# Performance work log

Hardware: AMD Instinct MI355X
Metric: run time of the kernel (lower is better)

Reference implementation:

```python
import jax, jax.numpy as jnp
import numpy as np

# Module config (mirrors SWTLayer(__init__) with dimensions=[64,64,16], kmax=[3,3], wavelet='db1')
DIMS = (64, 64)      # spatial sizes along axes 1,2
LEVELS = (6, 6)      # pywt.dwt_max_level(64, dec_len=2) == 6 (Haar)
KMAX = (3, 3)
NLIFT = 16
BATCH = 32


def swt_haar(x, level, axis):
    """pywt.swt(x, 'db1', level, trim_approx=True, norm=True) along `axis` (periodic).
    norm=True Haar level-j step s=2^(j-1): cA[i]=(a[i]+a[i+s])/2, cD[i]=(a[i]-a[i+s])/2.
    Returns concat([cA_n, cD_n, ..., cD_1]) along axis (length (level+1)*M)."""
    a = x
    details = []
    for j in range(level):
        s = 2 ** j
        sh = jnp.roll(a, -s, axis)   # a[i + s] (periodic)
        details.append((a - sh) * 0.5)
        a = (a + sh) * 0.5
    return jnp.concatenate([a] + details[::-1], axis=axis)


def iswt_haar(xt, level, axis):
    """pywt.iswt inverse of swt_haar: averages the two phase reconstructions per level."""
    bands = jnp.split(xt, level + 1, axis=axis)  # [cA_n, cD_n, ..., cD_1]
    a = bands[0]
    for j in range(level, 0, -1):
        cD = bands[level - j + 1]
        s = 2 ** (j - 1)
        a = 0.5 * ((a + cD) + jnp.roll(a - cD, s, axis))
    return a


def setup_inputs() -> dict:
    key = jax.random.key(0)
    k1, k2, k3 = jax.random.split(key, 3)
    x = jax.random.normal(k1, (BATCH, DIMS[0], DIMS[1], NLIFT), dtype=jnp.float32)
    W = jax.random.uniform(
        k2,
        (NLIFT, NLIFT, DIMS[0] * (LEVELS[0] + 1), DIMS[1] * (LEVELS[1] + 1)),
        dtype=jnp.float32,
    )
    b = jax.random.normal(k3, (NLIFT, NLIFT), dtype=jnp.float32)
    return {"x": x, "weights": W, "bias": b}


def reference(x, weights, bias):
    # forward SWT along each spatial axis -> (B, 448, 448, C)
    xt = x
    for i, L in enumerate(LEVELS):
        xt = swt_haar(xt, L, axis=i + 1)
    # truncate: zero wavenumber bands [kmax*M, level*M) along each spatial axis
    for i, (M, L, K) in enumerate(zip(DIMS, LEVELS, KMAX)):
        idx = (slice(None),) * (i + 1) + (slice(K * M, L * M),)
        xt = xt.at[idx].set(0.0)
    # per-location channel mixing: 'abcd,debc->abce'
    xt = jnp.einsum('abcd,debc->abce', xt, weights)
    # inverse SWT back to (B, 64, 64, C)
    out = xt
    for i, L in enumerate(LEVELS):
        out = iswt_haar(out, L, axis=i + 1)
    # skip path: F.linear(x, bias) == x @ bias.T
    return out + x @ bias.T
```

## Files before the change

### kernel.cpp

```cpp
#include <hip/hip_runtime.h>
#include <cstddef>
#include <cstdint>


#define X1_IDX(a,u,j,d) ((((size_t)(a)*256 + (u))*64 + (j))*16 + (d))

__global__ __launch_bounds__(64) void k_swt1(const float* __restrict__ x,
                                             float* __restrict__ X1) {
  const int tid = threadIdx.x;
  const int d = tid & 15, jl = tid >> 4;
  const int a = blockIdx.x;
  const int j = blockIdx.y * 4 + jl;
  __shared__ float col[64 * 64];
  const float* xp = x + ((size_t)a * 4096 + j) * 16 + d;
  float S = 0.f;
  for (int i = 0; i < 64; ++i) {
    float v = xp[(size_t)i * 1024];
    col[i * 64 + tid] = v;
    S += v;
  }
  const float cA = S * 0.015625f;
  float w4 = 0.f, w4b = 0.f;
  for (int t = 0; t < 16; ++t)  w4  += col[t * 64 + tid];
  for (int t = 16; t < 32; ++t) w4b += col[t * 64 + tid];
  float w5 = w4 + w4b;
  float* X1p = X1 + X1_IDX(a, 0, j, d);
  for (int u = 0; u < 64; ++u) {
    const float c0 = col[u * 64 + tid];
    const float c16 = col[((u + 16) & 63) * 64 + tid];
    const float c32 = col[((u + 32) & 63) * 64 + tid];
    const float c1 = col[((u + 1) & 63) * 64 + tid];
    X1p[(size_t)(u) * 1024]        = cA;
    X1p[(size_t)(64 + u) * 1024]   = w5 * 0.03125f - cA;
    X1p[(size_t)(128 + u) * 1024]  = (w4 - w4b) * 0.03125f;
    X1p[(size_t)(192 + u) * 1024]  = (c0 - c1) * 0.5f;
    w4 += c16 - c0;
    w4b += c32 - c16;
    w5 += c32 - c0;
  }
}

__global__ __launch_bounds__(64) void k_swt2(const float* __restrict__ X1,
                                             float* __restrict__ T, int a0) {
  const int tid = threadIdx.x;
  const int d = tid & 15, ul = tid >> 4;
  const int ac = blockIdx.x, a = a0 + ac;
  const int u = blockIdx.y * 4 + ul;
  __shared__ float col[64 * 64];
  const float* xp = X1 + X1_IDX(a, u, 0, d);
  float S = 0.f;
  for (int i = 0; i < 64; ++i) {
    float v = xp[i * 16];
    col[i * 64 + tid] = v;
    S += v;
  }
  const float cA = S * 0.015625f;
  float w4 = 0.f, w4b = 0.f;
  for (int t = 0; t < 16; ++t)  w4  += col[t * 64 + tid];
  for (int t = 16; t < 32; ++t) w4b += col[t * 64 + tid];
  float w5 = w4 + w4b;
  float* Tp = T + (((size_t)ac * 256 + u) * 256) * 16 + d;
  for (int v = 0; v < 64; ++v) {
    const float c0 = col[v * 64 + tid];
    const float c16 = col[((v + 16) & 63) * 64 + tid];
    const float c32 = col[((v + 32) & 63) * 64 + tid];
    const float c1 = col[((v + 1) & 63) * 64 + tid];
    Tp[(size_t)(v) * 16]        = cA;
    Tp[(size_t)(64 + v) * 16]   = w5 * 0.03125f - cA;
    Tp[(size_t)(128 + v) * 16]  = (w4 - w4b) * 0.03125f;
    Tp[(size_t)(192 + v) * 16]  = (c0 - c1) * 0.5f;
    w4 += c16 - c0;
    w4b += c32 - c16;
    w5 += c32 - c0;
  }
}

__global__ __launch_bounds__(256) void k_mix(float* __restrict__ T,
                                             const float* __restrict__ W, int na) {
  const int t = threadIdx.x;
  const int u = blockIdx.x;
  const int vc = blockIdx.y;
  const int kb = vc >> 2;
  const int v0 = vc * 16;
  const int ub = u >> 6;
  const int Brow = (ub == 3 ? 6 : ub) * 64 + (u & 63);
  const int Ccol = (kb == 3 ? 6 : kb) * 64 + (vc & 3) * 16;
  __shared__ float Wl[16 * 256];
  __shared__ float Tl[32 * 16 * 17];
  {
    const float* wp = W + (size_t)t * 200704 + (size_t)Brow * 448 + Ccol;
    #pragma unroll
    for (int i = 0; i < 16; i += 4) {
      float4 w4v = *(const float4*)(wp + i);
      Wl[(i + 0) * 256 + t] = w4v.x;
      Wl[(i + 1) * 256 + t] = w4v.y;
      Wl[(i + 2) * 256 + t] = w4v.z;
      Wl[(i + 3) * 256 + t] = w4v.w;
    }
  }
  for (int idx = t; idx < na * 256; idx += 256) {
    int a = idx >> 8, rem = idx & 255, vl = rem >> 4, dd = rem & 15;
    Tl[(a * 16 + vl) * 17 + dd] =
        T[(((size_t)a * 256 + u) * 256 + v0 + vl) * 16 + dd];
  }
  __syncthreads();
  const int e = t & 15, al = t >> 4;
  float y[2][16];
  for (int aa = 0; aa < na; aa += 16) {
    int a = aa + al;
    if (a < na) {
      for (int vl = 0; vl < 16; ++vl) {
        float acc = 0.f;
        #pragma unroll
        for (int dd = 0; dd < 16; ++dd)
          acc += Tl[(a * 16 + vl) * 17 + dd] * Wl[vl * 256 + dd * 16 + e];
        y[aa >> 4][vl] = acc;
      }
    }
  }
  __syncthreads();
  for (int aa = 0; aa < na; aa += 16) {
    int a = aa + al;
    if (a < na)
      for (int vl = 0; vl < 16; ++vl)
        T[(((size_t)a * 256 + u) * 256 + v0 + vl) * 16 + e] = y[aa >> 4][vl];
  }
}

__global__ __launch_bounds__(64) void k_iswt2(const float* __restrict__ T,
                                              float* __restrict__ Z1, int a0) {
  const int tid = threadIdx.x, e = tid & 15, ul = tid >> 4;
  const int ac = blockIdx.x, a = a0 + ac;
  const int u = blockIdx.y * 4 + ul;
  __shared__ float A[64 * 64], Bv[64 * 64];
  const float* Tp = T + (((size_t)ac * 256 + u) * 256) * 16 + e;
  for (int i = 0; i < 64; ++i) A[i * 64 + tid] = Tp[(size_t)i * 16];
  for (int i = 0; i < 64; ++i) {
    float D = Tp[(size_t)(64 + i) * 16];
    float D2 = Tp[(size_t)(64 + ((i - 32) & 63)) * 16];
    Bv[i * 64 + tid] = 0.5f * (A[i * 64 + tid] + D + A[((i - 32) & 63) * 64 + tid] - D2);
  }
  for (int i = 0; i < 64; ++i) {
    float D = Tp[(size_t)(128 + i) * 16];
    float D2 = Tp[(size_t)(128 + ((i - 16) & 63)) * 16];
    A[i * 64 + tid] = 0.5f * (Bv[i * 64 + tid] + D + Bv[((i - 16) & 63) * 64 + tid] - D2);
  }
  for (int i = 0; i < 64; ++i)
    Bv[i * 64 + tid] = 0.5f * (A[i * 64 + tid] + A[((i - 8) & 63) * 64 + tid]);
  for (int i = 0; i < 64; ++i)
    A[i * 64 + tid] = 0.5f * (Bv[i * 64 + tid] + Bv[((i - 4) & 63) * 64 + tid]);
  for (int i = 0; i < 64; ++i)
    Bv[i * 64 + tid] = 0.5f * (A[i * 64 + tid] + A[((i - 2) & 63) * 64 + tid]);
  float* Zp = Z1 + X1_IDX(a, u, 0, e);
  for (int i = 0; i < 64; ++i) {
    float D = Tp[(size_t)(192 + i) * 16];
    float D2 = Tp[(size_t)(192 + ((i - 1) & 63)) * 16];
    Zp[(size_t)i * 16] =
        0.5f * (Bv[i * 64 + tid] + D + Bv[((i - 1) & 63) * 64 + tid] - D2);
  }
}

__global__ __launch_bounds__(64) void k_iswt1(const float* __restrict__ Z1,
                                              const float* __restrict__ x,
                                              const float* __restrict__ bias,
                                              float* __restrict__ out) {
  const int tid = threadIdx.x, e = tid & 15, jl = tid >> 4;
  const int a = blockIdx.x, j = blockIdx.y * 4 + jl;
  __shared__ float A[64 * 64], Bv[64 * 64];
  __shared__ float bs[256];
  for (int i = tid; i < 256; i += 64) bs[i] = bias[i];
  __syncthreads();
  const float* Zp = Z1 + (size_t)a * 262144 + (size_t)j * 16 + e;
  for (int i = 0; i < 64; ++i) A[i * 64 + tid] = Zp[(size_t)i * 1024];
  for (int i = 0; i < 64; ++i) {
    float D = Zp[(size_t)(64 + i) * 1024];
    float D2 = Zp[(size_t)(64 + ((i - 32) & 63)) * 1024];
    Bv[i * 64 + tid] = 0.5f * (A[i * 64 + tid] + D + A[((i - 32) & 63) * 64 + tid] - D2);
  }
  for (int i = 0; i < 64; ++i) {
    float D = Zp[(size_t)(128 + i) * 1024];
    float D2 = Zp[(size_t)(128 + ((i - 16) & 63)) * 1024];
    A[i * 64 + tid] = 0.5f * (Bv[i * 64 + tid] + D + Bv[((i - 16) & 63) * 64 + tid] - D2);
  }
  for (int i = 0; i < 64; ++i)
    Bv[i * 64 + tid] = 0.5f * (A[i * 64 + tid] + A[((i - 8) & 63) * 64 + tid]);
  for (int i = 0; i < 64; ++i)
    A[i * 64 + tid] = 0.5f * (Bv[i * 64 + tid] + Bv[((i - 4) & 63) * 64 + tid]);
  for (int i = 0; i < 64; ++i)
    Bv[i * 64 + tid] = 0.5f * (A[i * 64 + tid] + A[((i - 2) & 63) * 64 + tid]);
  const float* xp = x + ((size_t)a * 4096 + j) * 16;
  float* op = out + ((size_t)a * 4096 + j) * 16 + e;
  for (int i = 0; i < 64; ++i) {
    float D = Zp[(size_t)(192 + i) * 1024];
    float D2 = Zp[(size_t)(192 + ((i - 1) & 63)) * 1024];
    float r = 0.5f * (Bv[i * 64 + tid] + D + Bv[((i - 1) & 63) * 64 + tid] - D2);
    float s = 0.f;
    #pragma unroll
    for (int dd = 0; dd < 16; ++dd) s += xp[(size_t)i * 1024 + dd] * bs[e * 16 + dd];
    op[(size_t)i * 1024] = r + s;
  }
}

extern "C" void kernel_launch(void* const* d_in, const int* in_sizes, int n_in,
                              void* d_out, int out_size, void* d_ws, size_t ws_size,
                              hipStream_t stream) {
  const float* x = (const float*)d_in[0];
  const float* W = (const float*)d_in[1];
  const float* bias = (const float*)d_in[2];
  float* out = (float*)d_out;
  float* X1 = (float*)d_ws;
  float* T = X1 + 8388608;
  int na = 32;
  while (na > 1 && ((size_t)8388608 + (size_t)na * 1048576) * 4 > ws_size) na >>= 1;

  k_swt1<<<dim3(32, 16), 64, 0, stream>>>(x, X1);
  for (int a0 = 0; a0 < 32; a0 += na) {
    k_swt2<<<dim3(na, 64), 64, 0, stream>>>(X1, T, a0);
    k_mix<<<dim3(256, 16), 256, 0, stream>>>(T, W, na);
    k_iswt2<<<dim3(na, 64), 64, 0, stream>>>(T, X1, a0);
  }
  k_iswt1<<<dim3(32, 16), 64, 0, stream>>>(X1, x, bias, out);
}
```

Measured before the change: 442.8 us.

## Fuse second-axis SWT, channel mixing and inverse SWT into one kernel

Replaces the swt2/mix/iswt2 kernel chain, and its batch-chunk loop, with a single kernel. Each block handles 8 batches for one u row and keeps the transformed 256x16 slab per batch in shared memory. This removes the round trip of the large T intermediate through global memory and the extra launches. The price is large per-thread register arrays, only half the threads active in the transform phases, and W being re-read by each of the 4 batch blocks.

```diff
diff --git a/kernel.cpp b/kernel.cpp
--- a/kernel.cpp
+++ b/kernel.cpp
@@ -40,123 +40,120 @@
   }
 }
 
-__global__ __launch_bounds__(64) void k_swt2(const float* __restrict__ X1,
-                                             float* __restrict__ T, int a0) {
-  const int tid = threadIdx.x;
-  const int d = tid & 15, ul = tid >> 4;
-  const int ac = blockIdx.x, a = a0 + ac;
-  const int u = blockIdx.y * 4 + ul;
-  __shared__ float col[64 * 64];
-  const float* xp = X1 + X1_IDX(a, u, 0, d);
-  float S = 0.f;
-  for (int i = 0; i < 64; ++i) {
-    float v = xp[i * 16];
-    col[i * 64 + tid] = v;
-    S += v;
-  }
-  const float cA = S * 0.015625f;
-  float w4 = 0.f, w4b = 0.f;
-  for (int t = 0; t < 16; ++t)  w4  += col[t * 64 + tid];
-  for (int t = 16; t < 32; ++t) w4b += col[t * 64 + tid];
-  float w5 = w4 + w4b;
-  float* Tp = T + (((size_t)ac * 256 + u) * 256) * 16 + d;
-  for (int v = 0; v < 64; ++v) {
-    const float c0 = col[v * 64 + tid];
-    const float c16 = col[((v + 16) & 63) * 64 + tid];
-    const float c32 = col[((v + 32) & 63) * 64 + tid];
-    const float c1 = col[((v + 1) & 63) * 64 + tid];
-    Tp[(size_t)(v) * 16]        = cA;
-    Tp[(size_t)(64 + v) * 16]   = w5 * 0.03125f - cA;
-    Tp[(size_t)(128 + v) * 16]  = (w4 - w4b) * 0.03125f;
-    Tp[(size_t)(192 + v) * 16]  = (c0 - c1) * 0.5f;
-    w4 += c16 - c0;
-    w4b += c32 - c16;
-    w5 += c32 - c0;
-  }
-}
-
-__global__ __launch_bounds__(256) void k_mix(float* __restrict__ T,
-                                             const float* __restrict__ W, int na) {
+#define APB 8
+#define TS_STRIDE 4104
+#define TS(a,v,d) ((a) * TS_STRIDE + (v) * 16 + (d))
+#define WL_STRIDE 264
+
+__global__ __launch_bounds__(256, 1) void k_fused(float* __restrict__ X1,
+                                                  const float* __restrict__ W) {
   const int t = threadIdx.x;
-  const int u = blockIdx.x;
-  const int vc = blockIdx.y;
-  const int kb = vc >> 2;
-  const int v0 = vc * 16;
+  const int a0 = blockIdx.x * APB;
+  const int u = blockIdx.y;
   const int ub = u >> 6;
   const int Brow = (ub == 3 ? 6 : ub) * 64 + (u & 63);
-  const int Ccol = (kb == 3 ? 6 : kb) * 64 + (vc & 3) * 16;
-  __shared__ float Wl[16 * 256];
-  __shared__ float Tl[32 * 16 * 17];
-  {
-    const float* wp = W + (size_t)t * 200704 + (size_t)Brow * 448 + Ccol;
-    #pragma unroll
-    for (int i = 0; i < 16; i += 4) {
-      float4 w4v = *(const float4*)(wp + i);
-      Wl[(i + 0) * 256 + t] = w4v.x;
-      Wl[(i + 1) * 256 + t] = w4v.y;
-      Wl[(i + 2) * 256 + t] = w4v.z;
-      Wl[(i + 3) * 256 + t] = w4v.w;
-    }
-  }
-  for (int idx = t; idx < na * 256; idx += 256) {
-    int a = idx >> 8, rem = idx & 255, vl = rem >> 4, dd = rem & 15;
-    Tl[(a * 16 + vl) * 17 + dd] =
-        T[(((size_t)a * 256 + u) * 256 + v0 + vl) * 16 + dd];
+  __shared__ float Ts[APB * TS_STRIDE];
+  __shared__ float Wl[16 * WL_STRIDE];
+
+  if (t < 128) {
+    const int a = t >> 4, d = t & 15;
+    const float* xp = X1 + X1_IDX(a0 + a, u, 0, d);
+    float raw[64];
+    float S = 0.f, w4 = 0.f, w4b = 0.f;
+#pragma unroll
+    for (int j = 0; j < 64; ++j) {
+      raw[j] = xp[j * 16];
+      S += raw[j];
+    }
+#pragma unroll
+    for (int j = 0; j < 16; ++j) w4 += raw[j];
+#pragma unroll
+    for (int j = 16; j < 32; ++j) w4b += raw[j];
+    const float cA = S * 0.015625f;
+    float w5 = w4 + w4b;
+#pragma unroll
+    for (int v = 0; v < 64; ++v) {
+      Ts[TS(a, v, d)]       = cA;
+      Ts[TS(a, 64 + v, d)]  = w5 * 0.03125f - cA;
+      Ts[TS(a, 128 + v, d)] = (w4 - w4b) * 0.03125f;
+      Ts[TS(a, 192 + v, d)] = (raw[v] - raw[(v + 1) & 63]) * 0.5f;
+      const float c0 = raw[v], c16 = raw[(v + 16) & 63], c32 = raw[(v + 32) & 63];
+      w4 += c16 - c0;
+      w4b += c32 - c16;
+      w5 += c32 - c0;
+    }
   }
   __syncthreads();
-  const int e = t & 15, al = t >> 4;
-  float y[2][16];
-  for (int aa = 0; aa < na; aa += 16) {
-    int a = aa + al;
-    if (a < na) {
-      for (int vl = 0; vl < 16; ++vl) {
-        float acc = 0.f;
-        #pragma unroll
-        for (int dd = 0; dd < 16; ++dd)
-          acc += Tl[(a * 16 + vl) * 17 + dd] * Wl[vl * 256 + dd * 16 + e];
-        y[aa >> 4][vl] = acc;
+
+  const int vl = t >> 4, e = t & 15;
+  const float* wbase = W + (size_t)t * 200704 + (size_t)Brow * 448;
+  for (int vg = 0; vg < 16; ++vg) {
+    const int kb = vg >> 2;
+    const int Ccol = (kb == 3 ? 6 : kb) * 64 + (vg & 3) * 16;
+    __syncthreads();
+    {
+      const float* wp = wbase + Ccol;
+#pragma unroll
+      for (int i = 0; i < 16; i += 4) {
+        float4 wv = *(const float4*)(wp + i);
+        Wl[(i + 0) * WL_STRIDE + t] = wv.x;
+        Wl[(i + 1) * WL_STRIDE + t] = wv.y;
+        Wl[(i + 2) * WL_STRIDE + t] = wv.z;
+        Wl[(i + 3) * WL_STRIDE + t] = wv.w;
       }
     }
+    __syncthreads();
+    const int v = vg * 16 + vl;
+    float wreg[16];
+#pragma unroll
+    for (int d = 0; d < 16; ++d) wreg[d] = Wl[vl * WL_STRIDE + d * 16 + e];
+#pragma unroll
+    for (int a = 0; a < APB; ++a) {
+      const float4 t0 = *(const float4*)&Ts[TS(a, v, 0)];
+      const float4 t1 = *(const float4*)&Ts[TS(a, v, 4)];
+      const float4 t2 = *(const float4*)&Ts[TS(a, v, 8)];
+      const float4 t3 = *(const float4*)&Ts[TS(a, v, 12)];
+      float acc = t0.x * wreg[0] + t0.y * wreg[1] + t0.z * wreg[2] + t0.w * wreg[3]
+                + t1.x * wreg[4] + t1.y * wreg[5] + t1.z * wreg[6] + t1.w * wreg[7]
+                + t2.x * wreg[8] + t2.y * wreg[9] + t2.z * wreg[10] + t2.w * wreg[11]
+                + t3.x * wreg[12] + t3.y * wreg[13] + t3.z * wreg[14] + t3.w * wreg[15];
+      Ts[TS(a, v, e)] = acc;
+    }
   }
   __syncthreads();
-  for (int aa = 0; aa < na; aa += 16) {
-    int a = aa + al;
-    if (a < na)
-      for (int vl = 0; vl < 16; ++vl)
-        T[(((size_t)a * 256 + u) * 256 + v0 + vl) * 16 + e] = y[aa >> 4][vl];
-  }
-}
-
-__global__ __launch_bounds__(64) void k_iswt2(const float* __restrict__ T,
-                                              float* __restrict__ Z1, int a0) {
-  const int tid = threadIdx.x, e = tid & 15, ul = tid >> 4;
-  const int ac = blockIdx.x, a = a0 + ac;
-  const int u = blockIdx.y * 4 + ul;
-  __shared__ float A[64 * 64], Bv[64 * 64];
-  const float* Tp = T + (((size_t)ac * 256 + u) * 256) * 16 + e;
-  for (int i = 0; i < 64; ++i) A[i * 64 + tid] = Tp[(size_t)i * 16];
-  for (int i = 0; i < 64; ++i) {
-    float D = Tp[(size_t)(64 + i) * 16];
-    float D2 = Tp[(size_t)(64 + ((i - 32) & 63)) * 16];
-    Bv[i * 64 + tid] = 0.5f * (A[i * 64 + tid] + D + A[((i - 32) & 63) * 64 + tid] - D2);
-  }
-  for (int i = 0; i < 64; ++i) {
-    float D = Tp[(size_t)(128 + i) * 16];
-    float D2 = Tp[(size_t)(128 + ((i - 16) & 63)) * 16];
-    A[i * 64 + tid] = 0.5f * (Bv[i * 64 + tid] + D + Bv[((i - 16) & 63) * 64 + tid] - D2);
-  }
-  for (int i = 0; i < 64; ++i)
-    Bv[i * 64 + tid] = 0.5f * (A[i * 64 + tid] + A[((i - 8) & 63) * 64 + tid]);
-  for (int i = 0; i < 64; ++i)
-    A[i * 64 + tid] = 0.5f * (Bv[i * 64 + tid] + Bv[((i - 4) & 63) * 64 + tid]);
-  for (int i = 0; i < 64; ++i)
-    Bv[i * 64 + tid] = 0.5f * (A[i * 64 + tid] + A[((i - 2) & 63) * 64 + tid]);
-  float* Zp = Z1 + X1_IDX(a, u, 0, e);
-  for (int i = 0; i < 64; ++i) {
-    float D = Tp[(size_t)(192 + i) * 16];
-    float D2 = Tp[(size_t)(192 + ((i - 1) & 63)) * 16];
-    Zp[(size_t)i * 16] =
-        0.5f * (Bv[i * 64 + tid] + D + Bv[((i - 1) & 63) * 64 + tid] - D2);
+
+  if (t < 128) {
+    const int a = t >> 4, ee = t & 15;
+    const float cA = Ts[TS(a, 0, ee)];
+    float d6[64];
+#pragma unroll
+    for (int i = 0; i < 64; ++i) d6[i] = Ts[TS(a, 64 + i, ee)];
+    float b6[64];
+#pragma unroll
+    for (int i = 0; i < 64; ++i) b6[i] = cA + 0.5f * (d6[i] - d6[(i - 32) & 63]);
+    float d5[64];
+#pragma unroll
+    for (int i = 0; i < 64; ++i) d5[i] = Ts[TS(a, 128 + i, ee)];
+    float a5[64];
+#pragma unroll
+    for (int i = 0; i < 64; ++i)
+      a5[i] = 0.5f * (b6[i] + d5[i] + b6[(i - 16) & 63] - d5[(i - 16) & 63]);
+    float b4[64];
+#pragma unroll
+    for (int i = 0; i < 64; ++i) b4[i] = 0.5f * (a5[i] + a5[(i - 8) & 63]);
+    float a3[64];
+#pragma unroll
+    for (int i = 0; i < 64; ++i) a3[i] = 0.5f * (b4[i] + b4[(i - 4) & 63]);
+    float b2[64];
+#pragma unroll
+    for (int i = 0; i < 64; ++i) b2[i] = 0.5f * (a3[i] + a3[(i - 2) & 63]);
+    float d1[64];
+#pragma unroll
+    for (int i = 0; i < 64; ++i) d1[i] = Ts[TS(a, 192 + i, ee)];
+    float* zp = X1 + X1_IDX(a0 + a, u, 0, ee);
+#pragma unroll
+    for (int j = 0; j < 64; ++j)
+      zp[j * 16] = 0.5f * (b2[j] + d1[j] + b2[(j - 1) & 63] - d1[(j - 1) & 63]);
   }
 }
 
@@ -195,7 +192,7 @@
     float D2 = Zp[(size_t)(192 + ((i - 1) & 63)) * 1024];
     float r = 0.5f * (Bv[i * 64 + tid] + D + Bv[((i - 1) & 63) * 64 + tid] - D2);
     float s = 0.f;
-    #pragma unroll
+#pragma unroll
     for (int dd = 0; dd < 16; ++dd) s += xp[(size_t)i * 1024 + dd] * bs[e * 16 + dd];
     op[(size_t)i * 1024] = r + s;
   }
@@ -209,15 +206,8 @@
   const float* bias = (const float*)d_in[2];
   float* out = (float*)d_out;
   float* X1 = (float*)d_ws;
-  float* T = X1 + 8388608;
-  int na = 32;
-  while (na > 1 && ((size_t)8388608 + (size_t)na * 1048576) * 4 > ws_size) na >>= 1;
 
   k_swt1<<<dim3(32, 16), 64, 0, stream>>>(x, X1);
-  for (int a0 = 0; a0 < 32; a0 += na) {
-    k_swt2<<<dim3(na, 64), 64, 0, stream>>>(X1, T, a0);
-    k_mix<<<dim3(256, 16), 256, 0, stream>>>(T, W, na);
-    k_iswt2<<<dim3(na, 64), 64, 0, stream>>>(T, X1, a0);
-  }
+  k_fused<<<dim3(4, 256), 256, 0, stream>>>(X1, W);
   k_iswt1<<<dim3(32, 16), 64, 0, stream>>>(X1, x, bias, out);
 }
```

Result: faster. 401.7 us (-9.3%).
